# Kernel optimization log

Measured on AMD Instinct MI355X. Metric: run time of the kernel, lower is better.

## Reference

```python
import jax, jax.numpy as jnp
import numpy as np

TAU = 0.07          # temperature
NUM_CLASSES = 1000  # label vocabulary size (used for bincount length)


def setup_inputs() -> dict:
    key = jax.random.key(0)
    kq, kk, ky = jax.random.split(key, 3)
    N, K, D = 8192, 8, 512
    q = jax.random.normal(kq, (N, D), dtype=jnp.float32)
    q = q / jnp.linalg.norm(q, axis=1, keepdims=True)          # L2-normalized anchors
    k = jax.random.normal(kk, (N, K, D), dtype=jnp.float32)
    k = k / jnp.linalg.norm(k, axis=2, keepdims=True)          # L2-normalized positives
    y = jax.random.randint(ky, (N,), 0, NUM_CLASSES, dtype=jnp.int32)
    return {"q": q, "k": k, "y": y}


def reference(q, k, y):
    # q: [N, D] anchors, k: [N, K, D] external positives, y: [N] labels
    N, K, D = k.shape
    neg_inf = jnp.float32(-jnp.inf)

    # similarities to external positives and within-batch, scaled by temperature
    k_sims = jnp.einsum('nd,nkd->nk', q, k) / TAU            # [N, K]
    batch_sims = jnp.matmul(q, q.T) / TAU                    # [N, N]

    same = y[:, None] == y[None, :]                          # [N, N] label equality
    eye = jnp.eye(N, dtype=bool)
    same_class_mask = same & ~eye                            # in-batch positives (excl. self)
    same_class_counts = same_class_mask.sum(axis=1) + K      # [N]

    # faithful to torch: multiply by mask then masked_fill(x == 0, -inf)
    batch_pos = batch_sims * same_class_mask
    batch_pos = jnp.where(batch_pos == 0, neg_inf, batch_pos)
    pos_sims = jnp.concatenate([k_sims, batch_pos], axis=1)  # [N, K+N]
    num = jax.scipy.special.logsumexp(pos_sims, axis=1)      # [N]

    y_counts = jnp.bincount(y, length=NUM_CLASSES)           # [C]
    neg_sims = batch_sims * (~same)
    neg_sims = jnp.where(neg_sims == 0, neg_inf, neg_sims)
    # class-frequency-weighted denominator (as in the original, no max-shift)
    den = jnp.log(jnp.sum(jnp.exp(neg_sims) / y_counts[y][None, :].astype(q.dtype), axis=1))

    loss = -(num - den) / same_class_counts.astype(q.dtype)
    return loss.mean()
```

## Files before the change

### kernel.cpp

```cpp
#include <hip/hip_runtime.h>
#include <hip/hip_fp8.h>
#include <stdint.h>

constexpr int N    = 8192;
constexpr int D    = 512;
constexpr int KEXT = 8;
constexpr int NCLS = 1000;
#define TAU_INV  14.285714285714285714f
#define SQRT_TI  3.7796447300922722f

typedef long   long2_t __attribute__((ext_vector_type(2)));
typedef float  f32x4   __attribute__((ext_vector_type(4)));

typedef __attribute__((address_space(1))) void gvoid;
typedef __attribute__((address_space(3))) void lvoid;

__device__ __forceinline__ uint32_t pack4_e4m3(float a, float b, float c, float d) {
    __hip_fp8_e4m3 A(a), B(b), C(c), D(d);
    return (uint32_t)A.__x | ((uint32_t)B.__x << 8) |
           ((uint32_t)C.__x << 16) | ((uint32_t)D.__x << 24);
}

__global__ void prep_k(const float* __restrict__ q, const int* __restrict__ y,
                       uint32_t* __restrict__ qf8, int* __restrict__ counts,
                       float* __restrict__ invy, float* __restrict__ pos,
                       float* __restrict__ neg) {
    const int b = blockIdx.x, tid = threadIdx.x;
    if (b == 0) {
        __shared__ int h[NCLS];
        for (int i = tid; i < NCLS; i += 256) h[i] = 0;
        __syncthreads();
        for (int i = tid; i < N; i += 256) atomicAdd(&h[y[i]], 1);
        __syncthreads();
        for (int i = tid; i < NCLS; i += 256) counts[i] = h[i];
        for (int i = tid; i < N; i += 256) invy[i] = 1.0f / (float)h[y[i]];
        return;
    }
    const int gid = (b - 1) * 256 + tid;
    const int row = gid >> 5;
    const int c   = gid & 31;
    const int ks2 = c >> 2, quad = c & 3;
    const float* src = q + (size_t)row * D + ks2 * 64 + quad * 8;
    float4 v0 = *reinterpret_cast<const float4*>(src);
    float4 v1 = *reinterpret_cast<const float4*>(src + 4);
    float4 v2 = *reinterpret_cast<const float4*>(src + 32);
    float4 v3 = *reinterpret_cast<const float4*>(src + 36);
    uint4 o;
    o.x = pack4_e4m3(v0.x * SQRT_TI, v0.y * SQRT_TI, v0.z * SQRT_TI, v0.w * SQRT_TI);
    o.y = pack4_e4m3(v1.x * SQRT_TI, v1.y * SQRT_TI, v1.z * SQRT_TI, v1.w * SQRT_TI);
    o.z = pack4_e4m3(v2.x * SQRT_TI, v2.y * SQRT_TI, v2.z * SQRT_TI, v2.w * SQRT_TI);
    o.w = pack4_e4m3(v3.x * SQRT_TI, v3.y * SQRT_TI, v3.z * SQRT_TI, v3.w * SQRT_TI);
    const int t = row >> 4, l15 = row & 15;
    reinterpret_cast<uint4*>(qf8)[(size_t)t * 512 + ks2 * 64 + quad * 16 + l15] = o;
    if (gid < N) { pos[gid] = 0.f; neg[gid] = 0.f; }
}

__global__ __launch_bounds__(256, 2) void gemm_k(
        const uint32_t* __restrict__ qf8,
        const int* __restrict__ y,
        const float* __restrict__ invy,
        float* __restrict__ pos_sum,
        float* __restrict__ neg_sum) {
    __shared__ long2_t Asl[4096];
    __shared__ int   yR[128];
    __shared__ float redP[2][128];
    __shared__ float redN[2][128];

    const int tid  = threadIdx.x;
    const int wave = tid >> 6;
    const int lane = tid & 63;
    const int quad = lane >> 4;
    const int l15  = lane & 15;

    const int ib     = blockIdx.x >> 3;
    const int jchunk = blockIdx.x & 7;
    const int ibase  = ib * 128;

    {
        const uint32_t* src = qf8 + (size_t)ib * 16384;
#pragma unroll
        for (int it = 0; it < 16; it++) {
            const int idx = it * 256 + tid;
            __builtin_amdgcn_global_load_lds((gvoid*)(src + idx * 4),
                                             (lvoid*)(Asl + idx), 16, 0, 0);
        }
    }
    if (tid < 128) yR[tid] = y[ibase + tid];
    __syncthreads();

    const int wr = (wave >> 1) * 64;
    const int wc = (wave & 1) * 64;
    const int half = wave & 1;

    int yi[16];
#pragma unroll
    for (int mi = 0; mi < 4; mi++)
#pragma unroll
        for (int r = 0; r < 4; r++)
            yi[mi * 4 + r] = yR[wr + mi * 16 + quad * 4 + r];

    float posp[16], negp[16];
#pragma unroll
    for (int e = 0; e < 16; e++) { posp[e] = 0.f; negp[e] = 0.f; }

    const long2_t* fb = reinterpret_cast<const long2_t*>(qf8);
    const long2_t* pB[4];
#pragma unroll
    for (int m = 0; m < 4; m++)
        pB[m] = fb + (size_t)(jchunk * 64 + (wc >> 4) + m) * 512 + lane;

    const int tA = wr >> 4;

    for (int jt = 0; jt < 8; jt++) {
        const int j0 = jchunk * 1024 + jt * 128;

        int   yjv[4];
        float icj[4];
#pragma unroll
        for (int mj = 0; mj < 4; mj++) {
            int jc = j0 + wc + mj * 16 + l15;
            yjv[mj] = y[jc];
            icj[mj] = invy[jc];
        }

        f32x4 acc[4][4];
#pragma unroll
        for (int a = 0; a < 4; a++)
#pragma unroll
            for (int c = 0; c < 4; c++) acc[a][c] = (f32x4)0.0f;

        long2_t af[2][4], bf[2][4];
#pragma unroll
        for (int m = 0; m < 4; m++) {
            af[0][m] = Asl[(tA + m) * 512 + lane];
            bf[0][m] = pB[m][0];
        }
#pragma unroll
        for (int ks2 = 0; ks2 < 8; ks2++) {
            const int cur = ks2 & 1, nxt = cur ^ 1;
            if (ks2 < 7) {
#pragma unroll
                for (int m = 0; m < 4; m++) {
                    af[nxt][m] = Asl[(tA + m) * 512 + (ks2 + 1) * 64 + lane];
                    bf[nxt][m] = pB[m][(ks2 + 1) * 64];
                }
            }
#pragma unroll
            for (int mi = 0; mi < 4; mi++)
#pragma unroll
                for (int mj = 0; mj < 4; mj++)
                    acc[mi][mj] = __builtin_amdgcn_mfma_f32_16x16x32_fp8_fp8(
                        af[cur][mi].x, bf[cur][mj].x, acc[mi][mj], 0, 0, 0);
#pragma unroll
            for (int mi = 0; mi < 4; mi++)
#pragma unroll
                for (int mj = 0; mj < 4; mj++)
                    acc[mi][mj] = __builtin_amdgcn_mfma_f32_16x16x32_fp8_fp8(
                        af[cur][mi].y, bf[cur][mj].y, acc[mi][mj], 0, 0, 0);
        }
#pragma unroll
        for (int m = 0; m < 4; m++) pB[m] += 4096;

#pragma unroll
        for (int mi = 0; mi < 4; mi++) {
#pragma unroll
            for (int r = 0; r < 4; r++) {
                const int e    = mi * 4 + r;
                const int irow = ibase + wr + mi * 16 + quad * 4 + r;
                const int myi  = yi[e];
                float ps = 0.f, ns = 0.f;
#pragma unroll
                for (int mj = 0; mj < 4; mj++) {
                    const int jcol = j0 + wc + mj * 16 + l15;
                    float a    = acc[mi][mj][r];
                    float ex   = __expf(a);
                    bool  nz   = (a != 0.0f);
                    bool  same = (myi == yjv[mj]);
                    ps += (same && (irow != jcol) && nz) ? ex : 0.0f;
                    ns += (!same && nz) ? ex * icj[mj] : 0.0f;
                }
                posp[e] += ps;
                negp[e] += ns;
            }
        }
    }

#pragma unroll
    for (int mi = 0; mi < 4; mi++) {
#pragma unroll
        for (int r = 0; r < 4; r++) {
            const int e = mi * 4 + r;
            float ps = posp[e], ns = negp[e];
#pragma unroll
            for (int off = 1; off < 16; off <<= 1) {
                ps += __shfl_xor(ps, off);
                ns += __shfl_xor(ns, off);
            }
            if (l15 == 0) {
                const int il = wr + mi * 16 + quad * 4 + r;
                redP[half][il] = ps;
                redN[half][il] = ns;
            }
        }
    }
    __syncthreads();
    if (tid < 128) {
        atomicAdd(&pos_sum[ibase + tid], redP[0][tid] + redP[1][tid]);
    } else if (tid < 256) {
        const int il = tid - 128;
        atomicAdd(&neg_sum[ibase + il], redN[0][il] + redN[1][il]);
    }
}

__global__ void finalize_k(const float* __restrict__ q, const float* __restrict__ kmat,
                           const int* __restrict__ y, const int* __restrict__ counts,
                           const float* __restrict__ pos_sum, const float* __restrict__ neg_sum,
                           float* __restrict__ loss) {
    const int wave = threadIdx.x >> 6, lane = threadIdx.x & 63;
    const int i = blockIdx.x * 4 + wave;

    const float4* q4 = reinterpret_cast<const float4*>(q) + (size_t)i * 128;
    const float4* k4 = reinterpret_cast<const float4*>(kmat) + (size_t)i * KEXT * 128;
    float4 qa = q4[lane], qb = q4[lane + 64];

    float esum = 0.f;
    for (int kk = 0; kk < KEXT; kk++) {
        float4 ka = k4[(size_t)kk * 128 + lane];
        float4 kb = k4[(size_t)kk * 128 + lane + 64];
        float p = qa.x * ka.x;
        p = fmaf(qa.y, ka.y, p); p = fmaf(qa.z, ka.z, p); p = fmaf(qa.w, ka.w, p);
        p = fmaf(qb.x, kb.x, p); p = fmaf(qb.y, kb.y, p);
        p = fmaf(qb.z, kb.z, p); p = fmaf(qb.w, kb.w, p);
#pragma unroll
        for (int off = 1; off < 64; off <<= 1) p += __shfl_xor(p, off);
        esum += __expf(p * TAU_INV);
    }
    if (lane == 0) {
        float num = logf(esum + pos_sum[i]);
        float den = logf(neg_sum[i]);
        float cnt = (float)(counts[y[i]] - 1 + KEXT);
        loss[i] = -(num - den) / cnt;
    }
}

__global__ void reduce_k(const float* __restrict__ loss, float* __restrict__ out) {
    __shared__ float part[16];
    int tid = threadIdx.x;
    float s = 0.f;
    for (int i = tid; i < N; i += 1024) s += loss[i];
#pragma unroll
    for (int off = 1; off < 64; off <<= 1) s += __shfl_xor(s, off);
    if ((tid & 63) == 0) part[tid >> 6] = s;
    __syncthreads();
    if (tid < 16) {
        float v = part[tid];
#pragma unroll
        for (int off = 1; off < 16; off <<= 1) v += __shfl_xor(v, off);
        if (tid == 0) out[0] = v / (float)N;
    }
}

extern "C" void kernel_launch(void* const* d_in, const int* in_sizes, int n_in,
                              void* d_out, int out_size, void* d_ws, size_t ws_size,
                              hipStream_t stream) {
    const float* q    = (const float*)d_in[0];
    const float* kmat = (const float*)d_in[1];
    const int*   y    = (const int*)d_in[2];
    float* out = (float*)d_out;

    char* ws = (char*)d_ws;
    uint32_t* qf8  = (uint32_t*)ws;
    int*   counts  = (int*)  (ws + 4194304);
    float* invy    = (float*)(ws + 4198400);
    float* pos     = (float*)(ws + 4231168);
    float* neg     = (float*)(ws + 4263936);
    float* loss    = (float*)(ws + 4296704);

    prep_k    <<<1 + (N * 32) / 256, 256, 0, stream>>>(q, y, qf8, counts, invy, pos, neg);
    gemm_k    <<<512, 256, 0, stream>>>(qf8, y, invy, pos, neg);
    finalize_k<<<N / 4, 256, 0, stream>>>(q, kmat, y, counts, pos, neg, loss);
    reduce_k  <<<1, 1024, 0, stream>>>(loss, out);
}
```

Before: 329.8 us.

## Use 16x16x128 scaled FP8 MFMA and fold log2e into prescale

```diff
diff --git a/kernel.cpp b/kernel.cpp
--- a/kernel.cpp
+++ b/kernel.cpp
@@ -7,10 +7,11 @@
 constexpr int KEXT = 8;
 constexpr int NCLS = 1000;
 #define TAU_INV  14.285714285714285714f
-#define SQRT_TI  3.7796447300922722f
+#define SC_L2    4.539816423767765f
 
 typedef long   long2_t __attribute__((ext_vector_type(2)));
 typedef float  f32x4   __attribute__((ext_vector_type(4)));
+typedef int    v8i     __attribute__((ext_vector_type(8)));
 
 typedef __attribute__((address_space(1))) void gvoid;
 typedef __attribute__((address_space(3))) void lvoid;
@@ -19,6 +20,15 @@
     __hip_fp8_e4m3 A(a), B(b), C(c), D(d);
     return (uint32_t)A.__x | ((uint32_t)B.__x << 8) |
            ((uint32_t)C.__x << 16) | ((uint32_t)D.__x << 24);
+}
+
+__device__ __forceinline__ f32x4 mfma128(long2_t alo, long2_t ahi,
+                                         long2_t blo, long2_t bhi, f32x4 c) {
+    union U { long2_t h[2]; v8i v; } A, B;
+    A.h[0] = alo; A.h[1] = ahi;
+    B.h[0] = blo; B.h[1] = bhi;
+    return __builtin_amdgcn_mfma_scale_f32_16x16x128_f8f6f4(
+        A.v, B.v, c, 0, 0, 0, 127, 0, 127);
 }
 
 __global__ void prep_k(const float* __restrict__ q, const int* __restrict__ y,
@@ -37,21 +47,21 @@
         return;
     }
     const int gid = (b - 1) * 256 + tid;
-    const int row = gid >> 5;
-    const int c   = gid & 31;
-    const int ks2 = c >> 2, quad = c & 3;
-    const float* src = q + (size_t)row * D + ks2 * 64 + quad * 8;
-    float4 v0 = *reinterpret_cast<const float4*>(src);
-    float4 v1 = *reinterpret_cast<const float4*>(src + 4);
-    float4 v2 = *reinterpret_cast<const float4*>(src + 32);
-    float4 v3 = *reinterpret_cast<const float4*>(src + 36);
-    uint4 o;
-    o.x = pack4_e4m3(v0.x * SQRT_TI, v0.y * SQRT_TI, v0.z * SQRT_TI, v0.w * SQRT_TI);
-    o.y = pack4_e4m3(v1.x * SQRT_TI, v1.y * SQRT_TI, v1.z * SQRT_TI, v1.w * SQRT_TI);
-    o.z = pack4_e4m3(v2.x * SQRT_TI, v2.y * SQRT_TI, v2.z * SQRT_TI, v2.w * SQRT_TI);
-    o.w = pack4_e4m3(v3.x * SQRT_TI, v3.y * SQRT_TI, v3.z * SQRT_TI, v3.w * SQRT_TI);
+    const int row = gid >> 4;
+    const int kb  = gid & 15;
+    const int ks4 = kb >> 2, quad = kb & 3;
+    const float* src = q + (size_t)row * D + kb * 32;
+    uint32_t o[8];
+#pragma unroll
+    for (int j = 0; j < 8; j++) {
+        float4 v = *reinterpret_cast<const float4*>(src + j * 4);
+        o[j] = pack4_e4m3(v.x * SC_L2, v.y * SC_L2, v.z * SC_L2, v.w * SC_L2);
+    }
     const int t = row >> 4, l15 = row & 15;
-    reinterpret_cast<uint4*>(qf8)[(size_t)t * 512 + ks2 * 64 + quad * 16 + l15] = o;
+    const size_t s16 = (size_t)((t * 4 + ks4) * 128) + quad * 16 + l15;
+    uint4* dst = reinterpret_cast<uint4*>(qf8);
+    dst[s16]      = make_uint4(o[0], o[1], o[2], o[3]);
+    dst[s16 + 64] = make_uint4(o[4], o[5], o[6], o[7]);
     if (gid < N) { pos[gid] = 0.f; neg[gid] = 0.f; }
 }
 
@@ -103,11 +113,11 @@
 #pragma unroll
     for (int e = 0; e < 16; e++) { posp[e] = 0.f; negp[e] = 0.f; }
 
-    const long2_t* fb = reinterpret_cast<const long2_t*>(qf8);
+    const long2_t* fbL = reinterpret_cast<const long2_t*>(qf8);
     const long2_t* pB[4];
 #pragma unroll
     for (int m = 0; m < 4; m++)
-        pB[m] = fb + (size_t)(jchunk * 64 + (wc >> 4) + m) * 512 + lane;
+        pB[m] = fbL + (size_t)(jchunk * 64 + (wc >> 4) + m) * 512 + lane;
 
     const int tA = wr >> 4;
 
@@ -129,34 +139,35 @@
 #pragma unroll
             for (int c = 0; c < 4; c++) acc[a][c] = (f32x4)0.0f;
 
-        long2_t af[2][4], bf[2][4];
+        long2_t blo[2][4], bhi[2][4];
 #pragma unroll
         for (int m = 0; m < 4; m++) {
-            af[0][m] = Asl[(tA + m) * 512 + lane];
-            bf[0][m] = pB[m][0];
-        }
-#pragma unroll
-        for (int ks2 = 0; ks2 < 8; ks2++) {
-            const int cur = ks2 & 1, nxt = cur ^ 1;
-            if (ks2 < 7) {
+            blo[0][m] = pB[m][0];
+            bhi[0][m] = pB[m][64];
+        }
+#pragma unroll
+        for (int ks4 = 0; ks4 < 4; ks4++) {
+            const int cur = ks4 & 1, nxt = cur ^ 1;
+            if (ks4 < 3) {
 #pragma unroll
                 for (int m = 0; m < 4; m++) {
-                    af[nxt][m] = Asl[(tA + m) * 512 + (ks2 + 1) * 64 + lane];
-                    bf[nxt][m] = pB[m][(ks2 + 1) * 64];
+                    blo[nxt][m] = pB[m][(ks4 + 1) * 128];
+                    bhi[nxt][m] = pB[m][(ks4 + 1) * 128 + 64];
                 }
             }
+            long2_t alo[4], ahi[4];
+#pragma unroll
+            for (int m = 0; m < 4; m++) {
+                alo[m] = Asl[((tA + m) * 4 + ks4) * 128 + lane];
+                ahi[m] = Asl[((tA + m) * 4 + ks4) * 128 + 64 + lane];
+            }
 #pragma unroll
             for (int mi = 0; mi < 4; mi++)
 #pragma unroll
                 for (int mj = 0; mj < 4; mj++)
-                    acc[mi][mj] = __builtin_amdgcn_mfma_f32_16x16x32_fp8_fp8(
-                        af[cur][mi].x, bf[cur][mj].x, acc[mi][mj], 0, 0, 0);
-#pragma unroll
-            for (int mi = 0; mi < 4; mi++)
-#pragma unroll
-                for (int mj = 0; mj < 4; mj++)
-                    acc[mi][mj] = __builtin_amdgcn_mfma_f32_16x16x32_fp8_fp8(
-                        af[cur][mi].y, bf[cur][mj].y, acc[mi][mj], 0, 0, 0);
+                    acc[mi][mj] = mfma128(alo[mi], ahi[mi],
+                                          blo[cur][mj], bhi[cur][mj],
+                                          acc[mi][mj]);
         }
 #pragma unroll
         for (int m = 0; m < 4; m++) pB[m] += 4096;
@@ -173,7 +184,7 @@
                 for (int mj = 0; mj < 4; mj++) {
                     const int jcol = j0 + wc + mj * 16 + l15;
                     float a    = acc[mi][mj][r];
-                    float ex   = __expf(a);
+                    float ex   = __builtin_amdgcn_exp2f(a);
                     bool  nz   = (a != 0.0f);
                     bool  same = (myi == yjv[mj]);
                     ps += (same && (irow != jcol) && nz) ? ex : 0.0f;
@@ -276,7 +287,7 @@
     float* neg     = (float*)(ws + 4263936);
     float* loss    = (float*)(ws + 4296704);
 
-    prep_k    <<<1 + (N * 32) / 256, 256, 0, stream>>>(q, y, qf8, counts, invy, pos, neg);
+    prep_k    <<<1 + (N * 16) / 256, 256, 0, stream>>>(q, y, qf8, counts, invy, pos, neg);
     gemm_k    <<<512, 256, 0, stream>>>(qf8, y, invy, pos, neg);
     finalize_k<<<N / 4, 256, 0, stream>>>(q, kmat, y, counts, pos, neg, loss);
     reduce_k  <<<1, 1024, 0, stream>>>(loss, out);
```

Result: faster. 312.5 us (-5.2%).
